# Performance work log

Hardware: AMD Instinct MI355X
Metric: run time of the kernel (lower is better)

Reference implementation:

```python
import jax, jax.numpy as jnp
import numpy as np

N_HEADS = 32
WINDOW = 128  # each query t attends keys max(0, t-window) .. t inclusive (window+1 keys)


def _sliding_window_attention(x, Wq, Wk, Wv, Wo, n_heads=N_HEADS, window=WINDOW):
    B, T, D = x.shape
    H, dk = n_heads, D // n_heads
    bs = window            # block size = window -> each query block sees exactly 2 key blocks
    assert T % bs == 0
    nb = T // bs

    def heads(y):  # [B,T,D] -> [B,H,T,dk]
        return y.reshape(B, T, H, dk).transpose(0, 2, 1, 3)

    q = heads(x @ Wq.T)
    k = heads(x @ Wk.T)
    v = heads(x @ Wv.T)

    # Block queries: [B,H,nb,bs,dk]
    qb = q.reshape(B, H, nb, bs, dk)
    # Pad one zero block in front of keys/values, then build per-block 2-block windows.
    zpad = jnp.zeros((B, H, bs, dk), dtype=x.dtype)
    kp = jnp.concatenate([zpad, k], axis=2).reshape(B, H, nb + 1, bs, dk)
    vp = jnp.concatenate([zpad, v], axis=2).reshape(B, H, nb + 1, bs, dk)
    kw = jnp.concatenate([kp[:, :, :-1], kp[:, :, 1:]], axis=3)  # [B,H,nb,2bs,dk]
    vw = jnp.concatenate([vp[:, :, :-1], vp[:, :, 1:]], axis=3)

    scale = 1.0 / np.sqrt(dk).astype(np.float32)
    # scores: [B,H,nb,bs,2bs]
    scores = jnp.einsum('bhnrd,bhncd->bhnrc', qb, kw) * scale

    # Banded causal mask. Query global pos = i*bs + r, key global pos = (i-1)*bs + c.
    i = jnp.arange(nb)[:, None, None]
    r = jnp.arange(bs)[None, :, None]
    c = jnp.arange(2 * bs)[None, None, :]
    dist = (bs + r) - c                       # qpos - keypos
    key_global = i * bs - bs + c
    valid = (dist >= 0) & (dist <= window) & (key_global >= 0)  # [nb,bs,2bs]

    scores = jnp.where(valid[None, None], scores, jnp.finfo(scores.dtype).min)
    probs = jax.nn.softmax(scores, axis=-1)
    out = jnp.einsum('bhnrc,bhncd->bhnrd', probs, vw)           # [B,H,nb,bs,dk]
    out = out.reshape(B, H, T, dk).transpose(0, 2, 1, 3).reshape(B, T, D)
    return out @ Wo.T


def setup_inputs() -> dict:
    key = jax.random.key(0)
    ks = jax.random.split(key, 5)
    B, T, D = 2, 4096, 2048
    w_std = 0.02
    return {
        'x':  jax.random.normal(ks[0], (B, T, D), dtype=jnp.float32),
        'Wq': jax.random.normal(ks[1], (D, D), dtype=jnp.float32) * w_std,
        'Wk': jax.random.normal(ks[2], (D, D), dtype=jnp.float32) * w_std,
        'Wv': jax.random.normal(ks[3], (D, D), dtype=jnp.float32) * w_std,
        'Wo': jax.random.normal(ks[4], (D, D), dtype=jnp.float32) * w_std,
    }


def reference(x, Wq, Wk, Wv, Wo):
    return _sliding_window_attention(x, Wq, Wk, Wv, Wo)
```

## Files before the change

kernel.cpp:

```cpp
#include <hip/hip_runtime.h>
#include <hip/hip_bf16.h>

typedef __attribute__((ext_vector_type(8))) short bf16x8;
typedef __attribute__((ext_vector_type(8))) unsigned short ushort8;
typedef __attribute__((ext_vector_type(4))) float f32x4;

#define MFMA16(a, b, c) __builtin_amdgcn_mfma_f32_16x16x32_bf16(a, b, c, 0, 0, 0)

__device__ __forceinline__ unsigned short f2bf(float x) {
    unsigned u = __builtin_bit_cast(unsigned, x);
    u += 0x7FFFu + ((u >> 16) & 1u);
    return (unsigned short)(u >> 16);
}

__device__ __forceinline__ void gload16(const void* g, void* l) {
    __builtin_amdgcn_global_load_lds((const __attribute__((address_space(1))) void*)g,
                                     (__attribute__((address_space(3))) void*)l, 16, 0, 0);
}

__device__ __forceinline__ void bar() {
    asm volatile("" ::: "memory");
    __builtin_amdgcn_s_barrier();
    asm volatile("" ::: "memory");
}

#define WAITL() do { asm volatile("s_waitcnt lgkmcnt(0)" ::: "memory"); \
                     __builtin_amdgcn_sched_barrier(0); } while (0)

__global__ void cvt_f32_bf16(const float* __restrict__ src, unsigned short* __restrict__ dst, int n8) {
    int stride = gridDim.x * blockDim.x;
    for (int i = blockIdx.x * blockDim.x + threadIdx.x; i < n8; i += stride) {
        const float4* s = reinterpret_cast<const float4*>(src) + (size_t)i * 2;
        float4 a = s[0], b = s[1];
        ushort8 o;
        o[0] = f2bf(a.x); o[1] = f2bf(a.y); o[2] = f2bf(a.z); o[3] = f2bf(a.w);
        o[4] = f2bf(b.x); o[5] = f2bf(b.y); o[6] = f2bf(b.z); o[7] = f2bf(b.w);
        *(reinterpret_cast<ushort8*>(dst) + i) = o;
    }
}

#define QUAD(mg, ng, bfv)                                                         \
    do {                                                                          \
        _Pragma("unroll") for (int mm = 0; mm < 4; ++mm)                          \
        _Pragma("unroll") for (int nn = 0; nn < 2; ++nn)                          \
        _Pragma("unroll") for (int kk = 0; kk < 2; ++kk)                          \
            acc[(mg) * 4 + mm][(ng) * 2 + nn] =                                   \
                MFMA16(af[mm][kk], bfv[nn][kk], acc[(mg) * 4 + mm][(ng) * 2 + nn]); \
    } while (0)

template <int STORE_F32>
__global__ __launch_bounds__(512, 2)
void gemm256(const unsigned short* __restrict__ A, const unsigned short* __restrict__ B,
             void* __restrict__ C, int M, int N, int K) {
    __shared__ char sm[131072];

    const int tid  = threadIdx.x;
    const int wid  = tid >> 6, lane = tid & 63;
    const int wr   = wid >> 2, wc = wid & 3;
    const int lrow = lane >> 4, lcol = lane & 15;

    const int flat = blockIdx.x;
    const int s = (flat & 7) * (gridDim.x >> 3) + (flat >> 3);
    const int nbn = N >> 8;
    const int bm = s / nbn, bn = s % nbn;

    const int srow = wid * 8 + (lane >> 3);
    const int scol = ((lane & 7) ^ ((lane >> 3) & 7)) * 8;
    const unsigned short* aS = A + (size_t)(bm * 256 + srow) * K + scol;
    const unsigned short* bS = B + (size_t)(bn * 256 + srow) * K + scol;
    const int ldsW = wid * 1024;

    auto stageA = [&](int d, int h, int t) {
#pragma unroll
        for (int q = 0; q < 2; ++q)
            gload16(aS + (size_t)(h * 128 + q * 64) * K + t * 64,
                    sm + d * 32768 + h * 16384 + ldsW + q * 8192);
    };
    auto stageB = [&](int d, int h, int t) {
#pragma unroll
        for (int q = 0; q < 2; ++q)
            gload16(bS + (size_t)(h * 128 + q * 64) * K + t * 64,
                    sm + 65536 + d * 32768 + h * 16384 + ldsW + q * 8192);
    };

    const int swz0 = (lrow * 16) ^ ((lcol & 7) << 4);
    const int swz1 = (64 + lrow * 16) ^ ((lcol & 7) << 4);
    const int ra = wr * 16 + lcol;
    const int rb = wc * 16 + lcol;

    bf16x8 af[4][2], bl[2][2], bh[2][2];
    auto loadA = [&](int d, int mg) {
#pragma unroll
        for (int mm = 0; mm < 4; ++mm) {
            af[mm][0] = *(const bf16x8*)(sm + d * 32768 + mg * 16384 + (mm * 32 + ra) * 128 + swz0);
            af[mm][1] = *(const bf16x8*)(sm + d * 32768 + mg * 16384 + (mm * 32 + ra) * 128 + swz1);
        }
    };
    auto loadB = [&](int d, int ng, bf16x8 (&bfv)[2][2]) {
#pragma unroll
        for (int nn = 0; nn < 2; ++nn) {
            bfv[nn][0] = *(const bf16x8*)(sm + 65536 + d * 32768 + ng * 16384 + (nn * 64 + rb) * 128 + swz0);
            bfv[nn][1] = *(const bf16x8*)(sm + 65536 + d * 32768 + ng * 16384 + (nn * 64 + rb) * 128 + swz1);
        }
    };

    f32x4 acc[8][4] = {};

    stageA(0, 0, 0); stageB(0, 0, 0); stageB(0, 1, 0); stageA(0, 1, 0);
    stageA(1, 0, 1); stageB(1, 0, 1); stageB(1, 1, 1);
    asm volatile("s_waitcnt vmcnt(6)" ::: "memory");
    bar();

    const int NI = K / 128;
#pragma unroll 1
    for (int i = 0; i < NI; ++i) {
        const int t0 = 2 * i;
        const bool last = (i == NI - 1);
        loadA(0, 0); loadB(0, 0, bl);
        stageA(1, 1, t0 + 1);
        bar(); WAITL();
        __builtin_amdgcn_s_setprio(1); QUAD(0, 0, bl); __builtin_amdgcn_s_setprio(0);
        bar();
        loadB(0, 1, bh);
        if (!last) stageA(0, 0, t0 + 2);
        bar(); WAITL();
        __builtin_amdgcn_s_setprio(1); QUAD(0, 1, bh); __builtin_amdgcn_s_setprio(0);
        bar();
        loadA(0, 1);
        if (!last) stageB(0, 0, t0 + 2);
        bar(); WAITL();
        __builtin_amdgcn_s_setprio(1); QUAD(1, 0, bl); __builtin_amdgcn_s_setprio(0);
        bar();
        if (!last) stageB(0, 1, t0 + 2);
        bar();
        __builtin_amdgcn_s_setprio(1); QUAD(1, 1, bh); __builtin_amdgcn_s_setprio(0);
        if (last) asm volatile("s_waitcnt vmcnt(0)" ::: "memory");
        else      asm volatile("s_waitcnt vmcnt(6)" ::: "memory");
        bar();
        loadA(1, 0); loadB(1, 0, bl);
        if (!last) stageA(0, 1, t0 + 2);
        bar(); WAITL();
        __builtin_amdgcn_s_setprio(1); QUAD(0, 0, bl); __builtin_amdgcn_s_setprio(0);
        bar();
        loadB(1, 1, bh);
        if (!last) stageA(1, 0, t0 + 3);
        bar(); WAITL();
        __builtin_amdgcn_s_setprio(1); QUAD(0, 1, bh); __builtin_amdgcn_s_setprio(0);
        bar();
        loadA(1, 1);
        if (!last) stageB(1, 0, t0 + 3);
        bar(); WAITL();
        __builtin_amdgcn_s_setprio(1); QUAD(1, 0, bl); __builtin_amdgcn_s_setprio(0);
        bar();
        if (!last) stageB(1, 1, t0 + 3);
        bar();
        __builtin_amdgcn_s_setprio(1); QUAD(1, 1, bh); __builtin_amdgcn_s_setprio(0);
        if (!last) asm volatile("s_waitcnt vmcnt(6)" ::: "memory");
        bar();
    }

    const size_t row0 = (size_t)bm * 256 + wr * 16 + lrow * 4;
    const int col0 = bn * 256 + wc * 16 + lcol;
#pragma unroll
    for (int m = 0; m < 8; ++m)
#pragma unroll
        for (int n = 0; n < 4; ++n)
#pragma unroll
            for (int r = 0; r < 4; ++r) {
                size_t row = row0 + m * 32 + r;
                size_t col = (size_t)col0 + n * 64;
                if (STORE_F32)
                    ((float*)C)[row * N + col] = acc[m][n][r];
                else
                    ((unsigned short*)C)[row * N + col] = f2bf(acc[m][n][r]);
            }
}

__global__ __launch_bounds__(256, 2)
void swa_attn(const unsigned short* __restrict__ Qb, const unsigned short* __restrict__ Kb,
              const unsigned short* __restrict__ Vb, unsigned short* __restrict__ Ob) {
    constexpr int T = 4096, D = 2048, BS = 128;
    __shared__ unsigned short vt[64][136];
    __shared__ unsigned short pl[4][32][136];

    const int i = blockIdx.x, h = blockIdx.y, b = blockIdx.z;
    const int tid = threadIdx.x;
    const int wid = tid >> 6, lane = tid & 63;
    const int lrow = lane >> 4, lcol = lane & 15;

    const size_t hoff = (size_t)h * 64;
    const unsigned short* qbase = Qb + (size_t)b * T * D + hoff;
    const unsigned short* kbase = Kb + (size_t)b * T * D + hoff;
    const unsigned short* vbase = Vb + (size_t)b * T * D + hoff;

    const int qr0 = i * BS + wid * 32;
    bf16x8 aq[2][2];
#pragma unroll
    for (int m = 0; m < 2; ++m)
#pragma unroll
        for (int kf = 0; kf < 2; ++kf)
            aq[m][kf] = *reinterpret_cast<const bf16x8*>(
                qbase + (size_t)(qr0 + m * 16 + lcol) * D + kf * 32 + lrow * 8);

    f32x4 oacc[2][4] = {};
    float mrun[2][4], lrun[2][4];
#pragma unroll
    for (int m = 0; m < 2; ++m)
#pragma unroll
        for (int r = 0; r < 4; ++r) { mrun[m][r] = -1e30f; lrun[m][r] = 0.f; }

    const int t0 = (i == 0) ? 1 : 0;
    for (int t = t0; t < 2; ++t) {
        const int kt0 = (i - 1) * BS + t * BS;

#pragma unroll
        for (int it = 0; it < 4; ++it) {
            int e = it * 2048 + tid * 8;
            int kr = e >> 6;
            int dc = e & 63;
            bf16x8 v = *reinterpret_cast<const bf16x8*>(vbase + (size_t)(kt0 + kr) * D + dc);
#pragma unroll
            for (int j = 0; j < 8; ++j) vt[dc + j][kr] = (unsigned short)v[j];
        }

        f32x4 s[2][8];
#pragma unroll
        for (int n = 0; n < 8; ++n) {
            const int ktr = kt0 + n * 16 + lcol;
            bf16x8 bk0 = *reinterpret_cast<const bf16x8*>(kbase + (size_t)ktr * D + lrow * 8);
            bf16x8 bk1 = *reinterpret_cast<const bf16x8*>(kbase + (size_t)ktr * D + 32 + lrow * 8);
#pragma unroll
            for (int m = 0; m < 2; ++m) {
                f32x4 a = {0.f, 0.f, 0.f, 0.f};
                a = MFMA16(aq[m][0], bk0, a);
                a = MFMA16(aq[m][1], bk1, a);
                s[m][n] = a;
            }
        }

#pragma unroll
        for (int m = 0; m < 2; ++m)
#pragma unroll
            for (int n = 0; n < 8; ++n)
#pragma unroll
                for (int r = 0; r < 4; ++r) {
                    int qr = wid * 32 + m * 16 + lrow * 4 + r;
                    int c  = t * BS + n * 16 + lcol;
                    bool valid = (c >= qr) && (c <= qr + BS);
                    s[m][n][r] = valid ? s[m][n][r] * 0.125f : -1e30f;
                }

#pragma unroll
        for (int m = 0; m < 2; ++m)
#pragma unroll
            for (int r = 0; r < 4; ++r) {
                float cm = s[m][0][r];
#pragma unroll
                for (int n = 1; n < 8; ++n) cm = fmaxf(cm, s[m][n][r]);
                cm = fmaxf(cm, __shfl_xor(cm, 1));
                cm = fmaxf(cm, __shfl_xor(cm, 2));
                cm = fmaxf(cm, __shfl_xor(cm, 4));
                cm = fmaxf(cm, __shfl_xor(cm, 8));
                float mnew = fmaxf(mrun[m][r], cm);
                float sf = __expf(mrun[m][r] - mnew);
                float rs = 0.f;
#pragma unroll
                for (int n = 0; n < 8; ++n) {
                    float p = __expf(s[m][n][r] - mnew);
                    s[m][n][r] = p;
                    rs += p;
                }
                rs += __shfl_xor(rs, 1);
                rs += __shfl_xor(rs, 2);
                rs += __shfl_xor(rs, 4);
                rs += __shfl_xor(rs, 8);
                lrun[m][r] = lrun[m][r] * sf + rs;
                mrun[m][r] = mnew;
#pragma unroll
                for (int nf = 0; nf < 4; ++nf) oacc[m][nf][r] *= sf;
            }

#pragma unroll
        for (int m = 0; m < 2; ++m)
#pragma unroll
            for (int n = 0; n < 8; ++n)
#pragma unroll
                for (int r = 0; r < 4; ++r)
                    pl[wid][m * 16 + lrow * 4 + r][n * 16 + lcol] = f2bf(s[m][n][r]);

        __syncthreads();

#pragma unroll
        for (int kf2 = 0; kf2 < 4; ++kf2) {
            bf16x8 ap0 = *reinterpret_cast<const bf16x8*>(&pl[wid][lcol][kf2 * 32 + lrow * 8]);
            bf16x8 ap1 = *reinterpret_cast<const bf16x8*>(&pl[wid][16 + lcol][kf2 * 32 + lrow * 8]);
#pragma unroll
            for (int nf = 0; nf < 4; ++nf) {
                bf16x8 bv = *reinterpret_cast<const bf16x8*>(&vt[nf * 16 + lcol][kf2 * 32 + lrow * 8]);
                oacc[0][nf] = MFMA16(ap0, bv, oacc[0][nf]);
                oacc[1][nf] = MFMA16(ap1, bv, oacc[1][nf]);
            }
        }
        __syncthreads();
    }

#pragma unroll
    for (int m = 0; m < 2; ++m)
#pragma unroll
        for (int r = 0; r < 4; ++r) {
            float inv = 1.f / lrun[m][r];
            int tok = i * BS + wid * 32 + m * 16 + lrow * 4 + r;
            unsigned short* orow = Ob + (size_t)(b * T + tok) * D + hoff;
#pragma unroll
            for (int nf = 0; nf < 4; ++nf)
                orow[nf * 16 + lcol] = f2bf(oacc[m][nf][r] * inv);
        }
}

extern "C" void kernel_launch(void* const* d_in, const int* in_sizes, int n_in,
                              void* d_out, int out_size, void* d_ws, size_t ws_size,
                              hipStream_t stream) {
    const float* x  = (const float*)d_in[0];
    const float* Wq = (const float*)d_in[1];
    const float* Wk = (const float*)d_in[2];
    const float* Wv = (const float*)d_in[3];
    const float* Wo = (const float*)d_in[4];

    constexpr int B = 2, T = 4096, D = 2048;
    constexpr int M = B * T;
    constexpr size_t XE = (size_t)M * D;
    constexpr size_t WE = (size_t)D * D;

    char* ws = (char*)d_ws;
    unsigned short* xb  = (unsigned short*)(ws);
    unsigned short* wqb = (unsigned short*)(ws + XE * 2);
    unsigned short* wkb = (unsigned short*)(ws + XE * 2 + WE * 2);
    unsigned short* wvb = (unsigned short*)(ws + XE * 2 + WE * 4);
    unsigned short* wob = (unsigned short*)(ws + XE * 2 + WE * 6);
    unsigned short* qb  = (unsigned short*)(ws + XE * 2 + WE * 8);
    unsigned short* kb  = (unsigned short*)(ws + XE * 4 + WE * 8);
    unsigned short* vb  = (unsigned short*)(ws + XE * 6 + WE * 8);
    unsigned short* ab  = (unsigned short*)(ws + XE * 8 + WE * 8);

    cvt_f32_bf16<<<2048, 256, 0, stream>>>(x,  xb,  (int)(XE / 8));
    cvt_f32_bf16<<<2048, 256, 0, stream>>>(Wq, wqb, (int)(WE / 8));
    cvt_f32_bf16<<<2048, 256, 0, stream>>>(Wk, wkb, (int)(WE / 8));
    cvt_f32_bf16<<<2048, 256, 0, stream>>>(Wv, wvb, (int)(WE / 8));
    cvt_f32_bf16<<<2048, 256, 0, stream>>>(Wo, wob, (int)(WE / 8));

    dim3 gg((M / 256) * (D / 256));
    gemm256<0><<<gg, 512, 0, stream>>>(xb, wqb, qb, M, D, D);
    gemm256<0><<<gg, 512, 0, stream>>>(xb, wkb, kb, M, D, D);
    gemm256<0><<<gg, 512, 0, stream>>>(xb, wvb, vb, M, D, D);

    swa_attn<<<dim3(32, 32, 2), 256, 0, stream>>>(qb, kb, vb, ab);

    gemm256<1><<<gg, 512, 0, stream>>>(ab, wob, d_out, M, D, D);
}
```

Before: 377.0 us.

## Fuse QKV projections into one GEMM and restructure sliding-window attention kernel

Result: faster. 358.3 us (-5.0%).

```diff
diff --git a/kernel.cpp b/kernel.cpp
--- a/kernel.cpp
+++ b/kernel.cpp
@@ -4,13 +4,23 @@
 typedef __attribute__((ext_vector_type(8))) short bf16x8;
 typedef __attribute__((ext_vector_type(8))) unsigned short ushort8;
 typedef __attribute__((ext_vector_type(4))) float f32x4;
+typedef __attribute__((ext_vector_type(2))) unsigned int u32x2;
 
 #define MFMA16(a, b, c) __builtin_amdgcn_mfma_f32_16x16x32_bf16(a, b, c, 0, 0, 0)
+#define CFENCE() asm volatile("" ::: "memory")
 
 __device__ __forceinline__ unsigned short f2bf(float x) {
     unsigned u = __builtin_bit_cast(unsigned, x);
     u += 0x7FFFu + ((u >> 16) & 1u);
     return (unsigned short)(u >> 16);
+}
+
+__device__ __forceinline__ float fexp2(float x) {
+#if __has_builtin(__builtin_amdgcn_exp2f)
+    return __builtin_amdgcn_exp2f(x);
+#else
+    return exp2f(x);
+#endif
 }
 
 __device__ __forceinline__ void gload16(const void* g, void* l) {
@@ -48,7 +58,7 @@
                 MFMA16(af[mm][kk], bfv[nn][kk], acc[(mg) * 4 + mm][(ng) * 2 + nn]); \
     } while (0)
 
-template <int STORE_F32>
+template <int MODE>
 __global__ __launch_bounds__(512, 2)
 void gemm256(const unsigned short* __restrict__ A, const unsigned short* __restrict__ B,
              void* __restrict__ C, int M, int N, int K) {
@@ -160,65 +170,72 @@
     }
 
     const size_t row0 = (size_t)bm * 256 + wr * 16 + lrow * 4;
-    const int col0 = bn * 256 + wc * 16 + lcol;
-#pragma unroll
-    for (int m = 0; m < 8; ++m)
-#pragma unroll
-        for (int n = 0; n < 4; ++n)
-#pragma unroll
-            for (int r = 0; r < 4; ++r) {
-                size_t row = row0 + m * 32 + r;
-                size_t col = (size_t)col0 + n * 64;
-                if (STORE_F32)
-                    ((float*)C)[row * N + col] = acc[m][n][r];
-                else
-                    ((unsigned short*)C)[row * N + col] = f2bf(acc[m][n][r]);
-            }
-}
-
-__global__ __launch_bounds__(256, 2)
+    if (MODE == 1) {
+        const int col0 = bn * 256 + wc * 16 + lcol;
+#pragma unroll
+        for (int m = 0; m < 8; ++m)
+#pragma unroll
+            for (int n = 0; n < 4; ++n)
+#pragma unroll
+                for (int r = 0; r < 4; ++r)
+                    ((float*)C)[(row0 + m * 32 + r) * N + col0 + n * 64] = acc[m][n][r];
+    } else {
+        const int seg = (bn * 256) >> 11;
+        const int coll = bn * 256 - seg * 2048 + wc * 16 + lcol;
+        unsigned short* out = (unsigned short*)C + (size_t)seg * 16777216ull;
+#pragma unroll
+        for (int m = 0; m < 8; ++m)
+#pragma unroll
+            for (int n = 0; n < 4; ++n)
+#pragma unroll
+                for (int r = 0; r < 4; ++r)
+                    out[(row0 + m * 32 + r) * 2048 + coll + n * 64] = f2bf(acc[m][n][r]);
+    }
+}
+
+__global__ __launch_bounds__(256, 3)
 void swa_attn(const unsigned short* __restrict__ Qb, const unsigned short* __restrict__ Kb,
               const unsigned short* __restrict__ Vb, unsigned short* __restrict__ Ob) {
-    constexpr int T = 4096, D = 2048, BS = 128;
+    constexpr int T = 4096, D = 2048;
+    constexpr float SC = 0.18033688011112042f;
+
     __shared__ unsigned short vt[64][136];
-    __shared__ unsigned short pl[4][32][136];
-
-    const int i = blockIdx.x, h = blockIdx.y, b = blockIdx.z;
-    const int tid = threadIdx.x;
-    const int wid = tid >> 6, lane = tid & 63;
-    const int lrow = lane >> 4, lcol = lane & 15;
-
-    const size_t hoff = (size_t)h * 64;
-    const unsigned short* qbase = Qb + (size_t)b * T * D + hoff;
-    const unsigned short* kbase = Kb + (size_t)b * T * D + hoff;
-    const unsigned short* vbase = Vb + (size_t)b * T * D + hoff;
-
-    const int qr0 = i * BS + wid * 32;
+    __shared__ unsigned short pls[4][32][40];
+
+    const int bid  = blockIdx.x;
+    const int flat = (bid & 7) * 256 + (bid >> 3);
+    const int i = flat & 31, h = (flat >> 5) & 31, b = flat >> 10;
+
+    const int tid = threadIdx.x, wid = tid >> 6, lane = tid & 63;
+    const int lcol = lane & 15, lrow = lane >> 4;
+
+    const unsigned short* qp = Qb + (size_t)b * T * D + h * 64;
+    const unsigned short* kp = Kb + (size_t)b * T * D + h * 64;
+    const unsigned short* vp = Vb + (size_t)b * T * D + h * 64;
+
+    const int t0 = (i == 0) ? 1 : 0;
+
+    const int q0 = i * 128 + wid * 32;
     bf16x8 aq[2][2];
 #pragma unroll
-    for (int m = 0; m < 2; ++m)
+    for (int qg = 0; qg < 2; ++qg)
 #pragma unroll
         for (int kf = 0; kf < 2; ++kf)
-            aq[m][kf] = *reinterpret_cast<const bf16x8*>(
-                qbase + (size_t)(qr0 + m * 16 + lcol) * D + kf * 32 + lrow * 8);
+            aq[qg][kf] = *(const bf16x8*)(qp + (size_t)(q0 + qg * 16 + lcol) * D + kf * 32 + lrow * 8);
 
     f32x4 oacc[2][4] = {};
-    float mrun[2][4], lrun[2][4];
-#pragma unroll
-    for (int m = 0; m < 2; ++m)
-#pragma unroll
-        for (int r = 0; r < 4; ++r) { mrun[m][r] = -1e30f; lrun[m][r] = 0.f; }
-
-    const int t0 = (i == 0) ? 1 : 0;
+    float mrun[2] = {-1e30f, -1e30f}, lrun[2] = {0.f, 0.f};
+
+#pragma unroll 1
     for (int t = t0; t < 2; ++t) {
-        const int kt0 = (i - 1) * BS + t * BS;
+        const int kt0 = (i - 1 + t) * 128;
 
 #pragma unroll
         for (int it = 0; it < 4; ++it) {
             int e = it * 2048 + tid * 8;
             int kr = e >> 6;
             int dc = e & 63;
-            bf16x8 v = *reinterpret_cast<const bf16x8*>(vbase + (size_t)(kt0 + kr) * D + dc);
+            bf16x8 v = *(const bf16x8*)(vp + (size_t)(kt0 + kr) * D + dc);
 #pragma unroll
             for (int j = 0; j < 8; ++j) vt[dc + j][kr] = (unsigned short)v[j];
         }
@@ -226,95 +243,98 @@
         f32x4 s[2][8];
 #pragma unroll
         for (int n = 0; n < 8; ++n) {
-            const int ktr = kt0 + n * 16 + lcol;
-            bf16x8 bk0 = *reinterpret_cast<const bf16x8*>(kbase + (size_t)ktr * D + lrow * 8);
-            bf16x8 bk1 = *reinterpret_cast<const bf16x8*>(kbase + (size_t)ktr * D + 32 + lrow * 8);
-#pragma unroll
-            for (int m = 0; m < 2; ++m) {
-                f32x4 a = {0.f, 0.f, 0.f, 0.f};
-                a = MFMA16(aq[m][0], bk0, a);
-                a = MFMA16(aq[m][1], bk1, a);
-                s[m][n] = a;
+            const unsigned short* krow = kp + (size_t)(kt0 + n * 16 + lcol) * D + lrow * 8;
+            bf16x8 k0 = *(const bf16x8*)(krow);
+            bf16x8 k1 = *(const bf16x8*)(krow + 32);
+            f32x4 z = {0.f, 0.f, 0.f, 0.f};
+            s[0][n] = MFMA16(k1, aq[0][1], MFMA16(k0, aq[0][0], z));
+            s[1][n] = MFMA16(k1, aq[1][1], MFMA16(k0, aq[1][0], z));
+        }
+
+#pragma unroll
+        for (int qg = 0; qg < 2; ++qg) {
+            const int q = wid * 32 + qg * 16 + lcol;
+#pragma unroll
+            for (int n = 0; n < 8; ++n) {
+                const int cb = t * 128 + n * 16 + lrow * 4 - q;
+#pragma unroll
+                for (int r = 0; r < 4; ++r)
+                    s[qg][n][r] = ((unsigned)(cb + r) <= 128u) ? s[qg][n][r] * SC : -1e30f;
             }
         }
 
 #pragma unroll
-        for (int m = 0; m < 2; ++m)
+        for (int qg = 0; qg < 2; ++qg) {
+            float cm = -1e30f;
 #pragma unroll
             for (int n = 0; n < 8; ++n)
 #pragma unroll
+                for (int r = 0; r < 4; ++r) cm = fmaxf(cm, s[qg][n][r]);
+            cm = fmaxf(cm, __shfl_xor(cm, 16));
+            cm = fmaxf(cm, __shfl_xor(cm, 32));
+            const float mn = fmaxf(mrun[qg], cm);
+            const float sf = fexp2(mrun[qg] - mn);
+            mrun[qg] = mn;
+            float rs = 0.f;
+#pragma unroll
+            for (int n = 0; n < 8; ++n)
+#pragma unroll
                 for (int r = 0; r < 4; ++r) {
-                    int qr = wid * 32 + m * 16 + lrow * 4 + r;
-                    int c  = t * BS + n * 16 + lcol;
-                    bool valid = (c >= qr) && (c <= qr + BS);
-                    s[m][n][r] = valid ? s[m][n][r] * 0.125f : -1e30f;
-                }
-
-#pragma unroll
-        for (int m = 0; m < 2; ++m)
-#pragma unroll
-            for (int r = 0; r < 4; ++r) {
-                float cm = s[m][0][r];
-#pragma unroll
-                for (int n = 1; n < 8; ++n) cm = fmaxf(cm, s[m][n][r]);
-                cm = fmaxf(cm, __shfl_xor(cm, 1));
-                cm = fmaxf(cm, __shfl_xor(cm, 2));
-                cm = fmaxf(cm, __shfl_xor(cm, 4));
-                cm = fmaxf(cm, __shfl_xor(cm, 8));
-                float mnew = fmaxf(mrun[m][r], cm);
-                float sf = __expf(mrun[m][r] - mnew);
-                float rs = 0.f;
-#pragma unroll
-                for (int n = 0; n < 8; ++n) {
-                    float p = __expf(s[m][n][r] - mnew);
-                    s[m][n][r] = p;
+                    float p = fexp2(s[qg][n][r] - mn);
+                    s[qg][n][r] = p;
                     rs += p;
                 }
-                rs += __shfl_xor(rs, 1);
-                rs += __shfl_xor(rs, 2);
-                rs += __shfl_xor(rs, 4);
-                rs += __shfl_xor(rs, 8);
-                lrun[m][r] = lrun[m][r] * sf + rs;
-                mrun[m][r] = mnew;
-#pragma unroll
-                for (int nf = 0; nf < 4; ++nf) oacc[m][nf][r] *= sf;
+            rs += __shfl_xor(rs, 16);
+            rs += __shfl_xor(rs, 32);
+            lrun[qg] = lrun[qg] * sf + rs;
+#pragma unroll
+            for (int nf = 0; nf < 4; ++nf) oacc[qg][nf] *= sf;
+        }
+
+        __syncthreads();
+
+#pragma unroll
+        for (int ks = 0; ks < 4; ++ks) {
+            CFENCE();
+#pragma unroll
+            for (int qg = 0; qg < 2; ++qg) {
+                unsigned short* prow = &pls[wid][qg * 16 + lcol][0];
+#pragma unroll
+                for (int r = 0; r < 4; ++r) {
+                    prow[4 * lrow + r]      = f2bf(s[qg][2 * ks][r]);
+                    prow[16 + 4 * lrow + r] = f2bf(s[qg][2 * ks + 1][r]);
+                }
             }
-
-#pragma unroll
-        for (int m = 0; m < 2; ++m)
-#pragma unroll
-            for (int n = 0; n < 8; ++n)
-#pragma unroll
-                for (int r = 0; r < 4; ++r)
-                    pl[wid][m * 16 + lrow * 4 + r][n * 16 + lcol] = f2bf(s[m][n][r]);
+            CFENCE();
+            WAITL();
+            bf16x8 pf0 = *(const bf16x8*)&pls[wid][lcol][lrow * 8];
+            bf16x8 pf1 = *(const bf16x8*)&pls[wid][16 + lcol][lrow * 8];
+#pragma unroll
+            for (int nf = 0; nf < 4; ++nf) {
+                bf16x8 av = *(const bf16x8*)&vt[nf * 16 + lcol][ks * 32 + lrow * 8];
+                oacc[0][nf] = MFMA16(av, pf0, oacc[0][nf]);
+                oacc[1][nf] = MFMA16(av, pf1, oacc[1][nf]);
+            }
+            CFENCE();
+        }
 
         __syncthreads();
-
-#pragma unroll
-        for (int kf2 = 0; kf2 < 4; ++kf2) {
-            bf16x8 ap0 = *reinterpret_cast<const bf16x8*>(&pl[wid][lcol][kf2 * 32 + lrow * 8]);
-            bf16x8 ap1 = *reinterpret_cast<const bf16x8*>(&pl[wid][16 + lcol][kf2 * 32 + lrow * 8]);
-#pragma unroll
-            for (int nf = 0; nf < 4; ++nf) {
-                bf16x8 bv = *reinterpret_cast<const bf16x8*>(&vt[nf * 16 + lcol][kf2 * 32 + lrow * 8]);
-                oacc[0][nf] = MFMA16(ap0, bv, oacc[0][nf]);
-                oacc[1][nf] = MFMA16(ap1, bv, oacc[1][nf]);
-            }
-        }
-        __syncthreads();
-    }
-
-#pragma unroll
-    for (int m = 0; m < 2; ++m)
-#pragma unroll
-        for (int r = 0; r < 4; ++r) {
-            float inv = 1.f / lrun[m][r];
-            int tok = i * BS + wid * 32 + m * 16 + lrow * 4 + r;
-            unsigned short* orow = Ob + (size_t)(b * T + tok) * D + hoff;
-#pragma unroll
-            for (int nf = 0; nf < 4; ++nf)
-                orow[nf * 16 + lcol] = f2bf(oacc[m][nf][r] * inv);
-        }
+    }
+
+#pragma unroll
+    for (int qg = 0; qg < 2; ++qg) {
+        const float inv = 1.f / lrun[qg];
+        const int tok = i * 128 + wid * 32 + qg * 16 + lcol;
+        unsigned short* orow = Ob + (size_t)(b * T + tok) * D + h * 64;
+#pragma unroll
+        for (int nf = 0; nf < 4; ++nf) {
+            unsigned o0 = (unsigned)f2bf(oacc[qg][nf][0] * inv) |
+                          ((unsigned)f2bf(oacc[qg][nf][1] * inv) << 16);
+            unsigned o1 = (unsigned)f2bf(oacc[qg][nf][2] * inv) |
+                          ((unsigned)f2bf(oacc[qg][nf][3] * inv) << 16);
+            *(u32x2*)(orow + nf * 16 + lrow * 4) = (u32x2){o0, o1};
+        }
+    }
 }
 
 extern "C" void kernel_launch(void* const* d_in, const int* in_sizes, int n_in,
@@ -348,12 +368,9 @@
     cvt_f32_bf16<<<2048, 256, 0, stream>>>(Wv, wvb, (int)(WE / 8));
     cvt_f32_bf16<<<2048, 256, 0, stream>>>(Wo, wob, (int)(WE / 8));
 
-    dim3 gg((M / 256) * (D / 256));
-    gemm256<0><<<gg, 512, 0, stream>>>(xb, wqb, qb, M, D, D);
-    gemm256<0><<<gg, 512, 0, stream>>>(xb, wkb, kb, M, D, D);
-    gemm256<0><<<gg, 512, 0, stream>>>(xb, wvb, vb, M, D, D);
-
-    swa_attn<<<dim3(32, 32, 2), 256, 0, stream>>>(qb, kb, vb, ab);
-
-    gemm256<1><<<gg, 512, 0, stream>>>(ab, wob, d_out, M, D, D);
-}
+    gemm256<2><<<dim3((M / 256) * (6144 / 256)), 512, 0, stream>>>(xb, wqb, qb, M, 6144, D);
+
+    swa_attn<<<dim3(2048), 256, 0, stream>>>(qb, kb, vb, ab);
+
+    gemm256<1><<<dim3((M / 256) * (D / 256)), 512, 0, stream>>>(ab, wob, d_out, M, D, D);
+}
```
